# Performance work log

Hardware: AMD Instinct MI355X
Metric: run time of the kernel (lower is better)

## Reference

```python
import jax, jax.numpy as jnp
import numpy as np

BN_EPS = 1e-5


def setup_inputs() -> dict:
    key = jax.random.key(0)
    ks = jax.random.split(key, 9)
    b, c, h, w = 8, 256, 256, 25
    p2_r = jax.random.normal(ks[0], (b, c, h, w), dtype=jnp.float32)
    # message-passing conv weight; scaled so the 25-step recurrence stays bounded
    W_msg = jax.random.normal(ks[1], (256, 256, 1, 9), dtype=jnp.float32) * 0.02
    bn_gamma = jax.random.uniform(ks[2], (256,), dtype=jnp.float32, minval=0.5, maxval=1.5)
    bn_beta = jax.random.normal(ks[3], (256,), dtype=jnp.float32) * 0.1
    bn_mean = jax.random.normal(ks[4], (256,), dtype=jnp.float32) * 0.1
    bn_var = jax.random.uniform(ks[5], (256,), dtype=jnp.float32, minval=0.5, maxval=1.5)
    W_up2 = jax.random.normal(ks[6], (256, 256, 3, 3), dtype=jnp.float32) * (1.0 / np.sqrt(256 * 9))
    W_conv = jax.random.normal(ks[7], (1, 256, 1, 1), dtype=jnp.float32) * (1.0 / np.sqrt(256))
    W_conv2 = jax.random.normal(ks[8], (1, 25, 1, 1), dtype=jnp.float32) * (1.0 / np.sqrt(25))
    return {"p2_r": p2_r, "W_msg": W_msg, "bn_gamma": bn_gamma, "bn_beta": bn_beta,
            "bn_mean": bn_mean, "bn_var": bn_var, "W_up2": W_up2,
            "W_conv": W_conv, "W_conv2": W_conv2}


def r_scnn(x, Wc, reverse):
    # x: [b,c,h,w]. The (1,9) conv with padding (0,4) on width-1 slices only
    # touches the kernel's center tap -> per-step 256x256 matvec recurrence.
    xs = jnp.moveaxis(x, 3, 0)  # [w,b,c,h]
    if reverse:
        xs = xs[::-1]

    def step(carry, xi):
        new = xi + jax.nn.relu(jnp.einsum('oc,bch->boh', Wc, carry))
        return new, new

    _, rest = jax.lax.scan(step, xs[0], xs[1:])
    out = jnp.concatenate([xs[:1], rest], axis=0)[::-1]  # source reverses output order
    return jnp.moveaxis(out, 0, 3)  # [b,c,h,w]


def batchnorm(x, gamma, beta, mean, var):
    inv = gamma / jnp.sqrt(var + BN_EPS)
    return x * inv[None, :, None, None] + (beta - mean * inv)[None, :, None, None]


def upsample_h2(x):
    # bilinear, align_corners=True, size=(2H, W): only height doubles
    b, c, H, W = x.shape
    nh = 2 * H
    pos = jnp.arange(nh, dtype=jnp.float32) * ((H - 1) / (nh - 1))
    i0 = jnp.floor(pos).astype(jnp.int32)
    i1 = jnp.minimum(i0 + 1, H - 1)
    t = (pos - i0.astype(jnp.float32))[None, None, :, None]
    return x[:, :, i0, :] * (1.0 - t) + x[:, :, i1, :] * t


def reference(p2_r, W_msg, bn_gamma, bn_beta, bn_mean, bn_var, W_up2, W_conv, W_conv2):
    Wc = W_msg[:, :, 0, 4]  # effective center tap of the (1,9) conv
    x = r_scnn(p2_r, Wc, reverse=False)
    x = jax.nn.relu(batchnorm(x, bn_gamma, bn_beta, bn_mean, bn_var))
    x = r_scnn(x, Wc, reverse=True)
    x = jax.nn.relu(batchnorm(x, bn_gamma, bn_beta, bn_mean, bn_var))
    x = upsample_h2(x)  # [b,256,2h,w]
    x = jax.lax.conv_general_dilated(x, W_up2, (1, 1), ((1, 1), (1, 1)),
                                     dimension_numbers=('NCHW', 'OIHW', 'NCHW'))
    x = upsample_h2(x)  # [b,256,4h,w]
    x = jnp.einsum('oc,bchw->bohw', W_conv[:, :, 0, 0], x)  # 1x1 conv 256->1
    x = upsample_h2(x)  # [b,1,8h,w]
    x = jnp.swapaxes(x, 1, 3)  # [b,w,8h,1]
    x = jnp.einsum('oc,bchw->bohw', W_conv2[:, :, 0, 0], x)  # 1x1 conv 25->1
    return jax.nn.sigmoid(x)  # [b,1,8h,1]
```

## Files before the change

kernel.cpp:

```cpp
#include <hip/hip_runtime.h>
#include <math.h>


#define NC 8

typedef __attribute__((ext_vector_type(8))) short bf16x8;
typedef __attribute__((ext_vector_type(4))) float f32x4;

__device__ __forceinline__ float relu_(float v) { return fmaxf(v, 0.f); }

__device__ __forceinline__ short f2bf(float f) {
  union { float f; unsigned u; } v; v.f = f;
  unsigned r = (v.u + 0x7fffu + ((v.u >> 16) & 1u)) >> 16;
  return (short)r;
}
__device__ __forceinline__ float bf2f(short s) {
  union { unsigned u; float f; } v;
  v.u = ((unsigned)(unsigned short)s) << 16;
  return v.f;
}
__device__ __forceinline__ unsigned cvtpk(float lo, float hi) {
  unsigned r;
  asm("v_cvt_pk_bf16_f32 %0, %1, %2" : "=v"(r) : "v"(lo), "v"(hi));
  return r;
}

__global__ __launch_bounds__(64) void k0_precompute(
    const float* __restrict__ Wmsg, const float* __restrict__ gamma,
    const float* __restrict__ beta, const float* __restrict__ mean,
    const float* __restrict__ var, const float* __restrict__ Wup2,
    const float* __restrict__ Wconv, const float* __restrict__ Wconv2,
    short* __restrict__ WcA, float* __restrict__ A, float* __restrict__ bnp)
{
  const int c = blockIdx.x;
  const int lane = threadIdx.x;

  for (int o = lane; o < 256; o += 64)
    WcA[o * 256 + c] = f2bf(Wmsg[(o * 256 + c) * 9 + 4]);

  const int gtid = c * 64 + lane;
  if (gtid < 256) {
    float inv = gamma[gtid] / sqrtf(var[gtid] + 1e-5f);
    bnp[gtid] = inv;
    bnp[256 + gtid] = beta[gtid] - mean[gtid] * inv;
  }

  float wacc[9];
#pragma unroll
  for (int q = 0; q < 9; ++q) wacc[q] = 0.f;
  for (int o = lane; o < 256; o += 64) {
    float cw = Wconv[o];
    const float* wp = Wup2 + (size_t)(o * 256 + c) * 9;
#pragma unroll
    for (int q = 0; q < 9; ++q) wacc[q] += cw * wp[q];
  }
#pragma unroll
  for (int q = 0; q < 9; ++q) {
    float v = wacc[q];
    v += __shfl_xor(v, 32, 64);
    v += __shfl_xor(v, 16, 64);
    v += __shfl_xor(v, 8, 64);
    v += __shfl_xor(v, 4, 64);
    v += __shfl_xor(v, 2, 64);
    v += __shfl_xor(v, 1, 64);
    wacc[q] = v;
  }
  if (lane == 0) {
    for (int dh = 0; dh < 3; ++dh)
      for (int j = 0; j < 25; ++j) {
        float a = 0.f;
        for (int dw = 0; dw < 3; ++dw) {
          int w = j + 1 - dw;
          if (w >= 0 && w < 25) a += wacc[dh * 3 + dw] * Wconv2[w];
        }
        A[(dh * 25 + j) * 256 + c] = a;
      }
  }
}

__global__ __launch_bounds__(512) void k2_fused(
    const float* __restrict__ X,
    const short* __restrict__ WcA,
    const float* __restrict__ A,
    const float* __restrict__ bnp,
    float* __restrict__ S)
{
  __shared__ short xslab[25 * 8 * 256];
  __shared__ short yz[2][16 * 256];
  __shared__ float red[8][8][3];
  const int tid = threadIdx.x;
  const int wave = tid >> 6;
  const int lane = tid & 63;
  const int n = lane & 15;
  const int nr = n & 7;
  const int g = lane >> 4;
  const bool isz = (n >= 8);
  const int col0 = blockIdx.x * NC;
  const int b = col0 >> 8, h0 = col0 & 255;
  const int obase = wave * 32;
  char* xs = (char*)xslab;
  char* smem = (char*)yz;

  {
    auto stage = [&](int cc, const float* src, int fbase) {
#pragma unroll
      for (int j = 0; j < 25; ++j) {
        float4 v = *(const float4*)(src + j * 4);
        float vv[4] = {v.x, v.y, v.z, v.w};
#pragma unroll
        for (int e = 0; e < 4; ++e) {
          int f = fbase + j * 4 + e;
          int rn = f / 25, w = f - rn * 25;
          *(short*)(xs + w * 4096 + rn * 512 + 2 * cc) = f2bf(vv[e]);
        }
      }
    };
    if (tid < 256) {
      stage(tid, X + ((size_t)(b * 256 + tid) * 256 + h0) * 25, 0);
    } else {
      int c2 = tid - 256;
      stage(c2, X + ((size_t)(b * 256 + c2) * 256 + h0) * 25 + 100, 100);
    }
  }

  f32x4 inv[2], addv[2];
#pragma unroll
  for (int t = 0; t < 2; ++t) {
    inv[t] = *(const f32x4*)(bnp + obase + t * 16 + g * 4);
    addv[t] = *(const f32x4*)(bnp + 256 + obase + t * 16 + g * 4);
  }

  bf16x8 af[2][8];
#pragma unroll
  for (int t = 0; t < 2; ++t)
#pragma unroll
    for (int kk = 0; kk < 8; ++kk)
      af[t][kk] = *(const bf16x8*)(WcA + (obase + t * 16 + n) * 256 + kk * 32 + g * 8);

  const int swz = nr << 4;
  int woff[2], roff[8], xoff[2];
#pragma unroll
  for (int t = 0; t < 2; ++t) {
    woff[t] = n * 512 + (((obase + t * 16 + g * 4) * 2) ^ swz);
    xoff[t] = nr * 512 + 2 * (obase + t * 16 + g * 4);
  }
#pragma unroll
  for (int kk = 0; kk < 8; ++kk)
    roff[kk] = n * 512 + ((kk * 64 + g * 16) ^ swz);

  __syncthreads();

  {
    uint2 xq0[2];
#pragma unroll
    for (int t = 0; t < 2; ++t) xq0[t] = *(const uint2*)(xs + xoff[t]);
    if (!isz) {
#pragma unroll
      for (int t = 0; t < 2; ++t)
        *(uint2*)(smem + woff[t]) = xq0[t];
    } else {
#pragma unroll
      for (int t = 0; t < 2; ++t) {
        float zr[4], t2r[4];
#pragma unroll
        for (int r = 0; r < 4; ++r) {
          short xb = (short)(r < 2 ? (r ? (xq0[t].x >> 16) : xq0[t].x)
                                   : (r & 1 ? (xq0[t].y >> 16) : xq0[t].y));
          float x = bf2f(xb);
          zr[r] = relu_(x * inv[t][r] + addv[t][r]);
          t2r[r] = relu_(zr[r] * inv[t][r] + addv[t][r]);
        }
        *(uint2*)(smem + woff[t]) = make_uint2(cvtpk(zr[0], zr[1]), cvtpk(zr[2], zr[3]));
        *(uint2*)(xs + xoff[t]) = make_uint2(cvtpk(t2r[0], t2r[1]), cvtpk(t2r[2], t2r[3]));
      }
    }
  }
  __syncthreads();

#pragma unroll 1
  for (int k = 1; k < 25; ++k) {
    const int cur = (k - 1) & 1, nxt = k & 1;

    uint2 xq[2];
    xq[0] = make_uint2(0u, 0u);
    xq[1] = make_uint2(0u, 0u);
    if (!isz) {
#pragma unroll
      for (int t = 0; t < 2; ++t)
        xq[t] = *(const uint2*)(xs + k * 4096 + xoff[t]);
    }

    bf16x8 bfr[8];
#pragma unroll
    for (int kk = 0; kk < 8; ++kk)
      bfr[kk] = *(const bf16x8*)(smem + cur * 8192 + roff[kk]);

    f32x4 acc0a = (f32x4){0.f, 0.f, 0.f, 0.f};
    f32x4 acc0b = (f32x4){0.f, 0.f, 0.f, 0.f};
    f32x4 acc1a = (f32x4){0.f, 0.f, 0.f, 0.f};
    f32x4 acc1b = (f32x4){0.f, 0.f, 0.f, 0.f};
#pragma unroll
    for (int kk = 0; kk < 4; ++kk) {
      acc0a = __builtin_amdgcn_mfma_f32_16x16x32_bf16(af[0][kk], bfr[kk], acc0a, 0, 0, 0);
      acc1a = __builtin_amdgcn_mfma_f32_16x16x32_bf16(af[1][kk], bfr[kk], acc1a, 0, 0, 0);
    }
#pragma unroll
    for (int kk = 4; kk < 8; ++kk) {
      acc0b = __builtin_amdgcn_mfma_f32_16x16x32_bf16(af[0][kk], bfr[kk], acc0b, 0, 0, 0);
      acc1b = __builtin_amdgcn_mfma_f32_16x16x32_bf16(af[1][kk], bfr[kk], acc1b, 0, 0, 0);
    }
    f32x4 acc0 = acc0a + acc0b;
    f32x4 acc1 = acc1a + acc1b;

#pragma unroll
    for (int t = 0; t < 2; ++t) {
      f32x4 acc = t ? acc1 : acc0;
      float xv[4];
      xv[0] = bf2f((short)xq[t].x);
      xv[1] = bf2f((short)(xq[t].x >> 16));
      xv[2] = bf2f((short)xq[t].y);
      xv[3] = bf2f((short)(xq[t].y >> 16));
      float sel[4], tt2[4];
#pragma unroll
      for (int r = 0; r < 4; ++r) {
        float cy = relu_(acc[r]);
        float ynew = xv[r] + cy;
        float t1 = relu_(ynew * inv[t][r] + addv[t][r]);
        float t1s = __shfl_xor(t1, 8);
        float znew = t1s + cy;
        tt2[r] = relu_(znew * inv[t][r] + addv[t][r]);
        sel[r] = isz ? znew : ynew;
      }
      *(uint2*)(smem + nxt * 8192 + woff[t]) =
          make_uint2(cvtpk(sel[0], sel[1]), cvtpk(sel[2], sel[3]));
      if (isz)
        *(uint2*)(xs + k * 4096 + xoff[t]) =
            make_uint2(cvtpk(tt2[0], tt2[1]), cvtpk(tt2[2], tt2[3]));
    }
    __syncthreads();
  }

  {
    const int c = tid & 255;
    const int kh = tid >> 8;
    float acc[8][3];
#pragma unroll
    for (int nn = 0; nn < 8; ++nn)
#pragma unroll
      for (int dh = 0; dh < 3; ++dh) acc[nn][dh] = 0.f;

    const int kbeg = kh ? 13 : 0, kend = kh ? 25 : 13;
    for (int k = kbeg; k < kend; ++k) {
      float a0 = A[(0 * 25 + 24 - k) * 256 + c];
      float a1 = A[(1 * 25 + 24 - k) * 256 + c];
      float a2 = A[(2 * 25 + 24 - k) * 256 + c];
#pragma unroll
      for (int nn = 0; nn < 8; ++nn) {
        float v = bf2f(*(const short*)(xs + k * 4096 + nn * 512 + 2 * c));
        acc[nn][0] = fmaf(a0, v, acc[nn][0]);
        acc[nn][1] = fmaf(a1, v, acc[nn][1]);
        acc[nn][2] = fmaf(a2, v, acc[nn][2]);
      }
    }
#pragma unroll
    for (int nn = 0; nn < 8; ++nn)
#pragma unroll
      for (int dh = 0; dh < 3; ++dh) {
        float v = acc[nn][dh];
        v += __shfl_xor(v, 1);
        v += __shfl_xor(v, 2);
        v += __shfl_xor(v, 4);
        v += __shfl_xor(v, 8);
        v += __shfl_xor(v, 16);
        v += __shfl_xor(v, 32);
        if (lane == 0) red[wave][nn][dh] = v;
      }
  }
  __syncthreads();
  if (tid < 24) {
    int nn = tid / 3, dh = tid % 3;
    float v = 0.f;
#pragma unroll
    for (int ww = 0; ww < 8; ++ww) v += red[ww][nn][dh];
    S[(size_t)(col0 + nn) * 3 + dh] = v;
  }
}

__global__ __launch_bounds__(256) void k3_outpre(
    const float* __restrict__ S, float* __restrict__ P)
{
  int idx = blockIdx.x * blockDim.x + threadIdx.x;
  if (idx >= 8 * 512) return;
  int b = idx >> 9, h = idx & 511;
  float acc = 0.f;
#pragma unroll
  for (int dh = 0; dh < 3; ++dh) {
    int hh = h + dh - 1;
    if (hh < 0 || hh >= 512) continue;
    float pos = hh * (255.0f / 511.0f);
    int i0 = (int)floorf(pos);
    int i1 = min(i0 + 1, 255);
    float t = pos - (float)i0;
    acc += (1.f - t) * S[(size_t)(b * 256 + i0) * 3 + dh]
         + t * S[(size_t)(b * 256 + i1) * 3 + dh];
  }
  P[idx] = acc;
}

__global__ __launch_bounds__(256) void k4_final(
    const float* __restrict__ P, float* __restrict__ out)
{
  int idx = blockIdx.x * blockDim.x + threadIdx.x;
  if (idx >= 8 * 2048) return;
  int b = idx >> 11, H = idx & 2047;
  const float* Pb = P + b * 512;

  float pos3 = H * (1023.0f / 2047.0f);
  int i3 = (int)floorf(pos3);
  int i3b = min(i3 + 1, 1023);
  float t3 = pos3 - (float)i3;

  float v[2];
#pragma unroll
  for (int q = 0; q < 2; ++q) {
    int i = q ? i3b : i3;
    float pos2 = i * (511.0f / 1023.0f);
    int i2 = (int)floorf(pos2);
    int i2b = min(i2 + 1, 511);
    float t2 = pos2 - (float)i2;
    v[q] = (1.f - t2) * Pb[i2] + t2 * Pb[i2b];
  }
  float val = (1.f - t3) * v[0] + t3 * v[1];
  out[idx] = 1.f / (1.f + expf(-val));
}

extern "C" void kernel_launch(void* const* d_in, const int* in_sizes, int n_in,
                              void* d_out, int out_size, void* d_ws, size_t ws_size,
                              hipStream_t stream) {
  (void)in_sizes; (void)n_in; (void)out_size; (void)ws_size;
  const float* p2r    = (const float*)d_in[0];
  const float* Wmsg   = (const float*)d_in[1];
  const float* gamma  = (const float*)d_in[2];
  const float* beta   = (const float*)d_in[3];
  const float* mean   = (const float*)d_in[4];
  const float* var    = (const float*)d_in[5];
  const float* Wup2   = (const float*)d_in[6];
  const float* Wconv  = (const float*)d_in[7];
  const float* Wconv2 = (const float*)d_in[8];
  float* out = (float*)d_out;

  float* ws = (float*)d_ws;
  size_t off = 0;
  short* WcA = (short*)(ws + off); off += 32768;
  float* Abuf = ws + off; off += 19200;
  float* bnp = ws + off;  off += 512;
  float* S = ws + off;    off += 6144;
  float* P = ws + off;    off += 4096;

  k0_precompute<<<256, 64, 0, stream>>>(Wmsg, gamma, beta, mean, var, Wup2,
                                        Wconv, Wconv2, WcA, Abuf, bnp);
  k2_fused<<<256, 512, 0, stream>>>(p2r, (const short*)WcA, Abuf, bnp, S);
  k3_outpre<<<16, 256, 0, stream>>>(S, P);
  k4_final<<<64, 256, 0, stream>>>(P, out);
}
```

Measured before the change: 64.68 us.

## Restructure input staging to coalesced per-wave loads with swizzled LDS slab

Input staging is reorganized so that the first 50 lanes of each wave each load float4s covering the contiguous 200-float row of one channel, for the wave's 32 channels. This replaces per-thread 100-float strided reads per channel. The LDS slab of bf16 values now uses an XOR swizzle that depends on the row and width index, and every reader and writer (recurrence loads, z-path writes, final reduction) applies the same swizzle. The aim is better global coalescing and fewer LDS bank conflicts on the scattered short stores. The cost is that 14 lanes per wave sit idle during staging, plus extra address arithmetic.

New measurement: 58.04 us. 10.3% less time.

```diff
diff --git a/kernel.cpp b/kernel.cpp
--- a/kernel.cpp
+++ b/kernel.cpp
@@ -102,24 +102,32 @@
   char* smem = (char*)yz;
 
   {
-    auto stage = [&](int cc, const float* src, int fbase) {
-#pragma unroll
-      for (int j = 0; j < 25; ++j) {
-        float4 v = *(const float4*)(src + j * 4);
-        float vv[4] = {v.x, v.y, v.z, v.w};
-#pragma unroll
-        for (int e = 0; e < 4; ++e) {
-          int f = fbase + j * 4 + e;
-          int rn = f / 25, w = f - rn * 25;
-          *(short*)(xs + w * 4096 + rn * 512 + 2 * cc) = f2bf(vv[e]);
+    const int L = lane;
+    if (L < 50) {
+      int base_[4], sx_[4];
+#pragma unroll
+      for (int e = 0; e < 4; ++e) {
+        int f = 4 * L + e;
+        int rn = f / 25, w = f - rn * 25;
+        base_[e] = w * 4096 + rn * 512;
+        sx_[e] = ((2 * rn + w) & 15) << 3;
+      }
+      const float* src0 = X + ((size_t)(b * 256 + obase) * 256 + h0) * 25 + 4 * L;
+#pragma unroll
+      for (int half = 0; half < 4; ++half) {
+        float4 v[8];
+#pragma unroll
+        for (int i = 0; i < 8; ++i)
+          v[i] = *(const float4*)(src0 + (size_t)(half * 8 + i) * 6400);
+#pragma unroll
+        for (int i = 0; i < 8; ++i) {
+          int c2 = (obase + half * 8 + i) * 2;
+          float vv[4] = {v[i].x, v[i].y, v[i].z, v[i].w};
+#pragma unroll
+          for (int e = 0; e < 4; ++e)
+            *(short*)(xs + base_[e] + (c2 ^ sx_[e])) = f2bf(vv[e]);
         }
       }
-    };
-    if (tid < 256) {
-      stage(tid, X + ((size_t)(b * 256 + tid) * 256 + h0) * 25, 0);
-    } else {
-      int c2 = tid - 256;
-      stage(c2, X + ((size_t)(b * 256 + c2) * 256 + h0) * 25 + 100, 100);
     }
   }
 
@@ -138,11 +146,11 @@
       af[t][kk] = *(const bf16x8*)(WcA + (obase + t * 16 + n) * 256 + kk * 32 + g * 8);
 
   const int swz = nr << 4;
-  int woff[2], roff[8], xoff[2];
+  int woff[2], roff[8], xb[2];
 #pragma unroll
   for (int t = 0; t < 2; ++t) {
     woff[t] = n * 512 + (((obase + t * 16 + g * 4) * 2) ^ swz);
-    xoff[t] = nr * 512 + 2 * (obase + t * 16 + g * 4);
+    xb[t] = nr * 512 + 2 * (obase + t * 16 + g * 4);
   }
 #pragma unroll
   for (int kk = 0; kk < 8; ++kk)
@@ -151,9 +159,10 @@
   __syncthreads();
 
   {
+    const int S0 = ((2 * nr) & 15) << 3;
     uint2 xq0[2];
 #pragma unroll
-    for (int t = 0; t < 2; ++t) xq0[t] = *(const uint2*)(xs + xoff[t]);
+    for (int t = 0; t < 2; ++t) xq0[t] = *(const uint2*)(xs + (xb[t] ^ S0));
     if (!isz) {
 #pragma unroll
       for (int t = 0; t < 2; ++t)
@@ -164,14 +173,15 @@
         float zr[4], t2r[4];
 #pragma unroll
         for (int r = 0; r < 4; ++r) {
-          short xb = (short)(r < 2 ? (r ? (xq0[t].x >> 16) : xq0[t].x)
-                                   : (r & 1 ? (xq0[t].y >> 16) : xq0[t].y));
-          float x = bf2f(xb);
+          short xbv = (short)(r < 2 ? (r ? (xq0[t].x >> 16) : xq0[t].x)
+                                    : (r & 1 ? (xq0[t].y >> 16) : xq0[t].y));
+          float x = bf2f(xbv);
           zr[r] = relu_(x * inv[t][r] + addv[t][r]);
           t2r[r] = relu_(zr[r] * inv[t][r] + addv[t][r]);
         }
         *(uint2*)(smem + woff[t]) = make_uint2(cvtpk(zr[0], zr[1]), cvtpk(zr[2], zr[3]));
-        *(uint2*)(xs + xoff[t]) = make_uint2(cvtpk(t2r[0], t2r[1]), cvtpk(t2r[2], t2r[3]));
+        *(uint2*)(xs + (xb[t] ^ S0)) =
+            make_uint2(cvtpk(t2r[0], t2r[1]), cvtpk(t2r[2], t2r[3]));
       }
     }
   }
@@ -180,6 +190,8 @@
 #pragma unroll 1
   for (int k = 1; k < 25; ++k) {
     const int cur = (k - 1) & 1, nxt = k & 1;
+    const int Sk = ((2 * nr + k) & 15) << 3;
+    const int kplane = k * 4096;
 
     uint2 xq[2];
     xq[0] = make_uint2(0u, 0u);
@@ -187,7 +199,7 @@
     if (!isz) {
 #pragma unroll
       for (int t = 0; t < 2; ++t)
-        xq[t] = *(const uint2*)(xs + k * 4096 + xoff[t]);
+        xq[t] = *(const uint2*)(xs + ((xb[t] + kplane) ^ Sk));
     }
 
     bf16x8 bfr[8];
@@ -234,7 +246,7 @@
       *(uint2*)(smem + nxt * 8192 + woff[t]) =
           make_uint2(cvtpk(sel[0], sel[1]), cvtpk(sel[2], sel[3]));
       if (isz)
-        *(uint2*)(xs + k * 4096 + xoff[t]) =
+        *(uint2*)(xs + ((xb[t] + kplane) ^ Sk)) =
             make_uint2(cvtpk(tt2[0], tt2[1]), cvtpk(tt2[2], tt2[3]));
     }
     __syncthreads();
@@ -256,7 +268,8 @@
       float a2 = A[(2 * 25 + 24 - k) * 256 + c];
 #pragma unroll
       for (int nn = 0; nn < 8; ++nn) {
-        float v = bf2f(*(const short*)(xs + k * 4096 + nn * 512 + 2 * c));
+        int Sp = ((2 * nn + k) & 15) << 3;
+        float v = bf2f(*(const short*)(xs + ((k * 4096 + nn * 512 + 2 * c) ^ Sp)));
         acc[nn][0] = fmaf(a0, v, acc[nn][0]);
         acc[nn][1] = fmaf(a1, v, acc[nn][1]);
         acc[nn][2] = fmaf(a2, v, acc[nn][2]);
```
